# Optimization experiments

Measured on AMD Instinct MI355X. Metric: run time of the kernel, lower is better.

Reference implementation:

```python
import jax, jax.numpy as jnp
import numpy as np

NEG = -1e9
EPS = 1e-5


def _layernorm(x, g, b):
    m = x.mean(-1, keepdims=True)
    v = ((x - m) ** 2).mean(-1, keepdims=True)
    return (x - m) / jnp.sqrt(v + EPS) * g + b


def _layer(h_aug, H_inc, mask_neg, W1, W1_hat, ctx1, W2, W2_hat, W3, g, b):
    # h_aug: (T, H), H_inc/mask_neg: (T, E)
    H = h_aug.shape[-1]
    scale = 1.0 / jnp.sqrt(jnp.asarray(H, h_aug.dtype))
    # Stage 1: node -> hyperedge attention
    proj_hat = h_aug @ W1_hat.T                       # (T, H)
    raw = (proj_hat * ctx1).sum(-1) * scale           # (T,)
    score = raw[:, None] + mask_neg                   # (T, E)
    alpha = jax.nn.softmax(score, axis=0) * H_inc     # (T, E)
    hyper = alpha.T @ (h_aug @ W1.T)                  # (E, H)
    # Stage 2: hyperedge -> node attention
    proj2_hat = hyper @ W2_hat.T                      # (E, H)
    score_ne = (h_aug @ W3.T) @ proj2_hat.T * scale + mask_neg  # (T, E)
    beta = jax.nn.softmax(score_ne, axis=1) * H_inc   # (T, E)
    out = beta @ (hyper @ W2.T)                       # (T, H)
    return _layernorm(out + h_aug, g, b)


def reference(node_emb, H_inc, membership, W1, W1_hat, ctx1, W2, W2_hat, W3, ln_g, ln_b, region_init):
    B, N, H = node_emb.shape
    R = region_init.shape[0]
    L = W1.shape[0]
    mask_neg = jnp.where(H_inc == 0, NEG, 0.0).astype(node_emb.dtype)
    counts = jax.ops.segment_sum(jnp.ones((N,), node_emb.dtype), membership, num_segments=R)
    safe_counts = jnp.maximum(counts, 1.0)

    def per_sample(h):  # h: (N, H)
        sums = jax.ops.segment_sum(h, membership, num_segments=R)     # (R, H)
        reg = jnp.where(counts[:, None] > 0, sums / safe_counts[:, None], 0.0)
        reg = reg + region_init
        h_aug = jnp.concatenate([h, reg], axis=0)                     # (N+R, H)
        for l in range(L):
            h_aug = _layer(h_aug, H_inc, mask_neg, W1[l], W1_hat[l], ctx1[l],
                           W2[l], W2_hat[l], W3[l], ln_g[l], ln_b[l])
        return h_aug[:N]

    return jax.vmap(per_sample)(node_emb)


def setup_inputs() -> dict:
    key = jax.random.key(0)
    ks = jax.random.split(key, 12)
    B, N, R, E, H, L = 4, 8000, 16, 1024, 128, 2
    T = N + R
    w_std = 1.0 / np.sqrt(H)
    node_emb = jax.random.normal(ks[0], (B, N, H), dtype=jnp.float32)
    H_inc = (jax.random.uniform(ks[1], (T, E)) < 0.05).astype(jnp.float32)
    membership = jax.random.randint(ks[2], (N,), 0, R, dtype=jnp.int32)
    W1 = jax.random.normal(ks[3], (L, H, H), dtype=jnp.float32) * w_std
    W1_hat = jax.random.normal(ks[4], (L, H, H), dtype=jnp.float32) * w_std
    ctx1 = jax.random.normal(ks[5], (L, H), dtype=jnp.float32) * 0.02
    W2 = jax.random.normal(ks[6], (L, H, H), dtype=jnp.float32) * w_std
    W2_hat = jax.random.normal(ks[7], (L, H, H), dtype=jnp.float32) * w_std
    W3 = jax.random.normal(ks[8], (L, H, H), dtype=jnp.float32) * w_std
    ln_g = jnp.ones((L, H), dtype=jnp.float32)
    ln_b = jnp.zeros((L, H), dtype=jnp.float32)
    region_init = jax.random.normal(ks[9], (R, H), dtype=jnp.float32) * 0.02
    return {"node_emb": node_emb, "H_inc": H_inc, "membership": membership,
            "W1": W1, "W1_hat": W1_hat, "ctx1": ctx1, "W2": W2, "W2_hat": W2_hat,
            "W3": W3, "ln_g": ln_g, "ln_b": ln_b, "region_init": region_init}
```

## Files before the change

### kernel.cpp

```cpp
#include <hip/hip_runtime.h>

#define HD 128
#define CAPE 768
#define MAXR 16
#define NB_RS 128
#define KSTR 136
#define VSTR 72

typedef unsigned short u16;
typedef unsigned long long u64;
typedef __attribute__((ext_vector_type(8))) short bf16x8;
typedef __attribute__((ext_vector_type(4))) float f32x4;
typedef __attribute__((ext_vector_type(4))) unsigned u32x4;

__device__ inline float b2f(unsigned u){ return __uint_as_float(u << 16); }
__device__ inline u16 f2b(float x){
  unsigned u = __float_as_uint(x);
  return (u16)((u + 0x7fffu + ((u >> 16) & 1u)) >> 16);
}

__device__ inline float waveSum(float v){ for(int o=32;o;o>>=1) v += __shfl_down(v,o); return v; }
__device__ inline float waveMax(float v){ for(int o=32;o;o>>=1) v = fmaxf(v,__shfl_down(v,o)); return v; }

__device__ inline float blockSum128(float v, float* red){
  int j = threadIdx.x;
  float s = waveSum(v);
  __syncthreads();
  if ((j & 63) == 0) red[j >> 6] = s;
  __syncthreads();
  return red[0] + red[1];
}
__device__ inline float blockMax128(float v, float* red){
  int j = threadIdx.x;
  float s = waveMax(v);
  __syncthreads();
  if ((j & 63) == 0) red[j >> 6] = s;
  __syncthreads();
  return fmaxf(red[0], red[1]);
}

__global__ void k_count(const int* __restrict__ memb, int N, int* __restrict__ counts){
  __shared__ int h[64];
  int tid = threadIdx.x;
  if (tid < 64) h[tid] = 0;
  __syncthreads();
  for (int t = blockIdx.x*blockDim.x + tid; t < N; t += gridDim.x*blockDim.x)
    atomicAdd(&h[memb[t]], 1);
  __syncthreads();
  if (tid < 64){ int v = h[tid]; if (v) atomicAdd(&counts[tid], v); }
}

__global__ __launch_bounds__(128) void k_regsum_fast(const float* __restrict__ node,
                        const int* __restrict__ memb, int N, int R,
                        float* __restrict__ partials){
  int b = blockIdx.y, j = threadIdx.x, blk = blockIdx.x;
  int nb = gridDim.x;
  int per = (N + nb - 1) / nb;
  int t0 = blk * per;
  int t1 = t0 + per; if (t1 > N) t1 = N;
  float acc[MAXR];
  #pragma unroll
  for (int i = 0; i < MAXR; ++i) acc[i] = 0.f;
  const float* base = node + (long)b*N*HD + j;
  for (int t = t0; t < t1; ++t){
    float v = base[(long)t*HD];
    int r = memb[t];
    #pragma unroll
    for (int i = 0; i < MAXR; ++i) acc[i] += (i == r) ? v : 0.f;
  }
  float* dst = partials + ((long)(b*nb + blk)*R)*HD + j;
  #pragma unroll
  for (int i = 0; i < MAXR; ++i)
    if (i < R) dst[(long)i*HD] = acc[i];
}

__global__ void k_regsum_lds(const float* __restrict__ node, const int* __restrict__ memb,
                             int N, int R, float* __restrict__ partials, int nb){
  extern __shared__ float acc[];
  int b = blockIdx.y, j = threadIdx.x;
  for (int r = 0; r < R; ++r) acc[r*HD + j] = 0.f;
  int per = (N + gridDim.x - 1) / gridDim.x;
  int t0 = blockIdx.x * per;
  int t1 = t0 + per; if (t1 > N) t1 = N;
  for (int t = t0; t < t1; ++t){
    int r = memb[t];
    acc[r*HD + j] += node[((long)b*N + t)*HD + j];
  }
  for (int r = 0; r < R; ++r)
    atomicAdd(&partials[((long)(b*nb)*R + r)*HD + j], acc[r*HD + j]);
}

__global__ void k_regfin(const float* __restrict__ partials, int nb, int redN,
                         const int* __restrict__ counts,
                         const float* __restrict__ rinit, float* __restrict__ h_aug,
                         int N, int R, int T, int B){
  int i = blockIdx.x*blockDim.x + threadIdx.x;
  if (i >= B*R*HD) return;
  int j = i % HD; int r = (i/HD) % R; int b = i/(HD*R);
  float s = 0.f;
  for (int blk = 0; blk < redN; ++blk)
    s += partials[((long)(b*nb + blk)*R + r)*HD + j];
  int c = counts[r];
  float v = (c > 0) ? s / (float)c : 0.f;
  v += rinit[r*HD + j];
  h_aug[((long)b*T + N + r)*HD + j] = v;
}

__global__ __launch_bounds__(128) void k_copyraw(const float* __restrict__ node,
                      const float* __restrict__ v, float* __restrict__ h_aug,
                      float* __restrict__ raw, int N, int T, float scale){
  int t = blockIdx.x, b = blockIdx.y, j = threadIdx.x;
  __shared__ float red[2];
  long rowb = (long)b*T + t;
  float x;
  if (t < N){ x = node[((long)b*N + t)*HD + j]; h_aug[rowb*HD + j] = x; }
  else      { x = h_aug[rowb*HD + j]; }
  float s = blockSum128(x * v[j], red);
  if (j == 0) raw[rowb] = s * scale;
}

__global__ __launch_bounds__(256) void k_maskbuild(const float* __restrict__ Hinc, int E, int MW,
                        u64* __restrict__ maskw){
  int t = blockIdx.x;
  int wv = threadIdx.x >> 6, lane = threadIdx.x & 63;
  const float* hrow = Hinc + (long)t*E;
  for (int w = wv; w < MW; w += 4){
    int e = w*64 + lane;
    bool f = (e < E) && (hrow[e] != 0.f);
    u64 mk = __ballot(f);
    if (lane == 0) maskw[(long)t*MW + w] = mk;
  }
}

__global__ __launch_bounds__(256) void k_colbuild2(const u64* __restrict__ maskw, int T, int MW,
                           u16* __restrict__ colidx, int* __restrict__ colcnt){
  int e = blockIdx.x;
  int w = e >> 6, bit = e & 63;
  int j = threadIdx.x;
  int lane = j & 63, wv = j >> 6;
  __shared__ int wsum[4];
  int c = 0;
  for (int base = 0; base < T; base += 256){
    int t = base + j;
    bool f = (t < T) && ((maskw[(long)t*MW + w] >> bit) & 1ull);
    u64 mk = __ballot(f);
    if (lane == 0) wsum[wv] = __popcll(mk);
    __syncthreads();
    int pre = 0;
    #pragma unroll
    for (int k = 0; k < 4; ++k) pre += (k < wv) ? wsum[k] : 0;
    int tot = wsum[0] + wsum[1] + wsum[2] + wsum[3];
    if (f){
      int pos = c + pre + (int)__popcll(mk & ((1ull << lane) - 1ull));
      if (pos < CAPE) colidx[(long)e*CAPE + pos] = (u16)t;
    }
    c += tot;
    __syncthreads();
  }
  if (j == 0) colcnt[e] = (c < CAPE) ? c : CAPE;
}

__global__ void k_ctxv(const float* __restrict__ ctx1, const float* __restrict__ W1h,
                       float* __restrict__ v){
  int l = blockIdx.x, k = threadIdx.x;
  float a = 0.f;
  for (int j = 0; j < HD; ++j) a += ctx1[l*HD + j] * W1h[((long)l*HD + j)*HD + k];
  v[l*HD + k] = a;
}

__global__ void k_mm128(const float* __restrict__ W2h, const float* __restrict__ W3,
                        float* __restrict__ MqT){
  int n = blockIdx.x, l = blockIdx.y, k = threadIdx.x;
  const float* A = W2h + (long)l*HD*HD;
  const float* Bm = W3 + (long)l*HD*HD;
  float s = 0.f;
  for (int j = 0; j < HD; ++j) s += A[(long)j*HD + n] * Bm[(long)j*HD + k];
  MqT[((long)l*HD + n)*HD + k] = s;
}

__global__ __launch_bounds__(256) void k_gemmM(const float* __restrict__ A,
                       const float* __restrict__ Wa, const float* __restrict__ Wb,
                       u16* __restrict__ Cb16, float* __restrict__ Cf32, int M, int zbase){
  int isB = ((blockIdx.y + zbase) == 0) ? 1 : 0;
  const float* W = isB ? Wa : Wb;
  __shared__ __align__(16) u16 Ws[128][KSTR];
  __shared__ __align__(16) u16 As[64][KSTR];
  int tid = threadIdx.x;
  int row0 = blockIdx.x * 64;
  for (int i = tid; i < 128*128; i += 256){
    int r = i >> 7, c = i & 127;
    Ws[r][c] = f2b(W[(long)r*HD + c]);
  }
  for (int i = tid; i < 64*128; i += 256){
    int r = i >> 7, c = i & 127;
    int gr = row0 + r;
    As[r][c] = (gr < M) ? f2b(A[(long)gr*HD + c]) : (u16)0;
  }
  __syncthreads();

  int wave = tid >> 6, lane = tid & 63;
  int wr0 = wave * 16;
  int frow = lane & 15;
  int koff = (lane >> 4) * 8;
  f32x4 acc[8];
  #pragma unroll
  for (int f = 0; f < 8; ++f) acc[f] = (f32x4){0.f,0.f,0.f,0.f};

  #pragma unroll
  for (int ks = 0; ks < 4; ++ks){
    int kc = ks*32 + koff;
    bf16x8 av = *(const bf16x8*)&As[wr0 + frow][kc];
    #pragma unroll
    for (int f = 0; f < 8; ++f){
      bf16x8 bv = *(const bf16x8*)&Ws[f*16 + frow][kc];
      acc[f] = __builtin_amdgcn_mfma_f32_16x16x32_bf16(av, bv, acc[f], 0, 0, 0);
    }
  }

  int orow = wr0 + (lane >> 4) * 4;
  #pragma unroll
  for (int f = 0; f < 8; ++f){
    int col = f*16 + frow;
    #pragma unroll
    for (int i = 0; i < 4; ++i){
      int gr = row0 + orow + i;
      if (gr < M){
        if (isB) Cb16[(long)gr*HD + col] = f2b(acc[f][i]);
        else     Cf32[(long)gr*HD + col] = acc[f][i];
      }
    }
  }
}

__global__ __launch_bounds__(256) void k_gemmW2T(const float* __restrict__ W2,
                       const u16* __restrict__ hyb, u16* __restrict__ hw2t, int E){
  int b = blockIdx.y;
  int e0 = blockIdx.x * 64;
  __shared__ __align__(16) u16 As[128][KSTR];
  __shared__ __align__(16) u16 Bs[64][KSTR];
  int tid = threadIdx.x;
  for (int i = tid; i < 128*128; i += 256){
    int r = i >> 7, c = i & 127;
    As[r][c] = f2b(W2[(long)r*HD + c]);
  }
  {
    int er = tid >> 2, q = (tid & 3)*32;
    if (e0 + er < E){
      const uint4* src = (const uint4*)(hyb + ((long)b*E + e0 + er)*HD + q);
      uint4 w0 = src[0], w1 = src[1], w2 = src[2], w3 = src[3];
      *(uint4*)&Bs[er][q]    = w0;
      *(uint4*)&Bs[er][q+8]  = w1;
      *(uint4*)&Bs[er][q+16] = w2;
      *(uint4*)&Bs[er][q+24] = w3;
    } else {
      uint4 z = {0,0,0,0};
      *(uint4*)&Bs[er][q] = z; *(uint4*)&Bs[er][q+8] = z;
      *(uint4*)&Bs[er][q+16] = z; *(uint4*)&Bs[er][q+24] = z;
    }
  }
  __syncthreads();
  int wv = tid >> 6, lane = tid & 63;
  int lc = lane & 15, lg = lane >> 4;
  f32x4 acc[2][4];
  #pragma unroll
  for (int mt=0;mt<2;++mt)
    #pragma unroll
    for (int nf=0;nf<4;++nf) acc[mt][nf] = (f32x4){0.f,0.f,0.f,0.f};
  #pragma unroll
  for (int mt=0;mt<2;++mt){
    int hr = wv*32 + mt*16 + lc;
    #pragma unroll
    for (int ks=0;ks<4;++ks){
      bf16x8 av = *(const bf16x8*)&As[hr][ks*32 + lg*8];
      #pragma unroll
      for (int nf=0;nf<4;++nf){
        bf16x8 bv = *(const bf16x8*)&Bs[nf*16+lc][ks*32 + lg*8];
        acc[mt][nf] = __builtin_amdgcn_mfma_f32_16x16x32_bf16(av, bv, acc[mt][nf], 0,0,0);
      }
    }
  }
  #pragma unroll
  for (int mt=0;mt<2;++mt){
    #pragma unroll
    for (int nf=0;nf<4;++nf){
      #pragma unroll
      for (int i=0;i<4;++i){
        int h = wv*32 + mt*16 + lg*4 + i;
        int e = e0 + nf*16 + lc;
        if (e < E) hw2t[((long)b*HD + h)*E + e] = f2b(acc[mt][nf][i]);
      }
    }
  }
}

__global__ __launch_bounds__(128) void k_edge(int swz, const float* __restrict__ raw,
                      const u16* __restrict__ proj1b,
                      const int* __restrict__ colcnt, const u16* __restrict__ colidx,
                      u16* __restrict__ hyb, int T, int E){
  int bi = blockIdx.x;
  int b, e;
  if (swz){ int x = bi & 7; b = x >> 1; e = ((bi >> 3) << 1) | (x & 1); }
  else    { b = bi / E; e = bi - b*E; }
  int j = threadIdx.x;
  __shared__ float red[2];
  __shared__ float wls[CAPE];
  __shared__ int   tls[CAPE];
  int c = colcnt[e]; if (c > CAPE) c = CAPE;
  const u16* ci = colidx + (long)e*CAPE;
  const float* rawb = raw + (long)b*T;
  long orow = ((long)b*E + e)*HD + j;
  if (c <= 0){ hyb[orow] = 0; return; }
  float lm = -1e30f;
  for (int i = j; i < c; i += 128){
    int t = ci[i];
    float v = rawb[t];
    tls[i] = t;
    wls[i] = v;
    lm = fmaxf(lm, v);
  }
  float m = blockMax128(lm, red);
  float lz = 0.f;
  for (int i = j; i < c; i += 128){
    float w = __expf(wls[i] - m);
    wls[i] = w;
    lz += w;
  }
  float Z = blockSum128(lz, red);
  float invZ = 1.f / Z;
  const u16* pb = proj1b + (long)b*T*HD + j;
  float a0=0.f,a1=0.f,a2=0.f,a3=0.f;
  int i = 0;
  for (; i + 4 <= c; i += 4){
    a0 += wls[i]   * b2f(pb[(long)tls[i]  *HD]);
    a1 += wls[i+1] * b2f(pb[(long)tls[i+1]*HD]);
    a2 += wls[i+2] * b2f(pb[(long)tls[i+2]*HD]);
    a3 += wls[i+3] * b2f(pb[(long)tls[i+3]*HD]);
  }
  for (; i < c; ++i) a0 += wls[i] * b2f(pb[(long)tls[i]*HD]);
  hyb[orow] = f2b(((a0+a1)+(a2+a3)) * invZ);
}

__global__ __launch_bounds__(256) void k_flash(
      const float* __restrict__ qt, const u16* __restrict__ hyb, const u16* __restrict__ hw2t,
      const u64* __restrict__ maskw,
      const float* __restrict__ lng, const float* __restrict__ lnb,
      const float* __restrict__ vnext, float* __restrict__ rawnext, int writeRaw,
      float* __restrict__ h_aug, float* __restrict__ out,
      int T, int E, int N, int writeOut, float scale){
  int b = blockIdx.y;
  int t0 = blockIdx.x * 64;
  int tid = threadIdx.x;
  int wv = tid >> 6, lane = tid & 63;
  int lc = lane & 15, lg = lane >> 4;

  __shared__ __align__(16) u16 Ks[64][KSTR];
  __shared__ __align__(16) u16 Vs[128][VSTR];

  int qrow = t0 + wv*16 + lc;
  bf16x8 qf[4];
  if (qrow < T){
    const float* qr = qt + ((long)b*T + qrow)*HD + lg*8;
    #pragma unroll
    for (int ks = 0; ks < 4; ++ks){
      const float4* q4 = (const float4*)(qr + ks*32);
      float4 a = q4[0], cc = q4[1];
      bf16x8 v;
      v[0]=(short)f2b(a.x);  v[1]=(short)f2b(a.y);  v[2]=(short)f2b(a.z);  v[3]=(short)f2b(a.w);
      v[4]=(short)f2b(cc.x); v[5]=(short)f2b(cc.y); v[6]=(short)f2b(cc.z); v[7]=(short)f2b(cc.w);
      qf[ks] = v;
    }
  } else {
    #pragma unroll
    for (int ks = 0; ks < 4; ++ks) qf[ks] = (bf16x8){0,0,0,0,0,0,0,0};
  }

  float m_s = -1e30f, l_s = 0.f;
  f32x4 Oa[8];
  #pragma unroll
  for (int f=0;f<8;++f) Oa[f] = (f32x4){0.f,0.f,0.f,0.f};

  const u16* hyB = hyb + (long)b*E*HD;
  const u16* vtB = hw2t + (long)b*HD*E;
  int MW = (E + 63) >> 6;
  int ntile = (E + 63) / 64;

  int kr = tid >> 2, kq = (tid & 3)*32;
  int vh = tid >> 1, vo = (tid & 1)*32;

  uint4 kreg0, kreg1, kreg2, kreg3, vreg0, vreg1, vreg2, vreg3;
  const uint4 zz = make_uint4(0u,0u,0u,0u);

  {
    int e0 = 0;
    if (e0 + kr < E){
      const uint4* s = (const uint4*)(hyB + (long)(e0+kr)*HD + kq);
      kreg0=s[0]; kreg1=s[1]; kreg2=s[2]; kreg3=s[3];
    } else { kreg0=zz; kreg1=zz; kreg2=zz; kreg3=zz; }
    if (e0 + vo + 31 < E){
      const uint4* s = (const uint4*)(vtB + (long)vh*E + e0 + vo);
      vreg0=s[0]; vreg1=s[1]; vreg2=s[2]; vreg3=s[3];
    } else {
      union { uint4 v[4]; u16 s[32]; } u;
      #pragma unroll
      for (int k=0;k<32;++k){ int e=e0+vo+k; u.s[k] = (e<E)? vtB[(long)vh*E+e] : (u16)0; }
      vreg0=u.v[0]; vreg1=u.v[1]; vreg2=u.v[2]; vreg3=u.v[3];
    }
  }

  for (int et = 0; et < ntile; ++et){
    *(uint4*)&Ks[kr][kq]    = kreg0;
    *(uint4*)&Ks[kr][kq+8]  = kreg1;
    *(uint4*)&Ks[kr][kq+16] = kreg2;
    *(uint4*)&Ks[kr][kq+24] = kreg3;
    {
      int eb0 = vo;        int ne0 = eb0>>4; int ka0 = (ne0>>1)*32 + ((eb0>>2)&3)*8 + (ne0&1)*4;
      int eb1 = vo + 8;    int ne1 = eb1>>4; int ka1 = (ne1>>1)*32 + ((eb1>>2)&3)*8 + (ne1&1)*4;
      int eb2 = vo + 16;   int ne2 = eb2>>4; int ka2 = (ne2>>1)*32 + ((eb2>>2)&3)*8 + (ne2&1)*4;
      int eb3 = vo + 24;   int ne3 = eb3>>4; int ka3 = (ne3>>1)*32 + ((eb3>>2)&3)*8 + (ne3&1)*4;
      *(uint2*)&Vs[vh][ka0]   = make_uint2(vreg0.x, vreg0.y);
      *(uint2*)&Vs[vh][ka0+8] = make_uint2(vreg0.z, vreg0.w);
      *(uint2*)&Vs[vh][ka1]   = make_uint2(vreg1.x, vreg1.y);
      *(uint2*)&Vs[vh][ka1+8] = make_uint2(vreg1.z, vreg1.w);
      *(uint2*)&Vs[vh][ka2]   = make_uint2(vreg2.x, vreg2.y);
      *(uint2*)&Vs[vh][ka2+8] = make_uint2(vreg2.z, vreg2.w);
      *(uint2*)&Vs[vh][ka3]   = make_uint2(vreg3.x, vreg3.y);
      *(uint2*)&Vs[vh][ka3+8] = make_uint2(vreg3.z, vreg3.w);
    }
    __syncthreads();
    if (et + 1 < ntile){
      int e0 = (et+1)*64;
      if (e0 + kr < E){
        const uint4* s = (const uint4*)(hyB + (long)(e0+kr)*HD + kq);
        kreg0=s[0]; kreg1=s[1]; kreg2=s[2]; kreg3=s[3];
      } else { kreg0=zz; kreg1=zz; kreg2=zz; kreg3=zz; }
      if (e0 + vo + 31 < E){
        const uint4* s = (const uint4*)(vtB + (long)vh*E + e0 + vo);
        vreg0=s[0]; vreg1=s[1]; vreg2=s[2]; vreg3=s[3];
      } else {
        union { uint4 v[4]; u16 s[32]; } u;
        #pragma unroll
        for (int k=0;k<32;++k){ int e=e0+vo+k; u.s[k] = (e<E)? vtB[(long)vh*E+e] : (u16)0; }
        vreg0=u.v[0]; vreg1=u.v[1]; vreg2=u.v[2]; vreg3=u.v[3];
      }
    }

    u64 mw = (qrow < T) ? maskw[(long)qrow*MW + et] : 0ull;

    f32x4 accS[4];
    #pragma unroll
    for (int ne=0;ne<4;++ne) accS[ne] = (f32x4){0.f,0.f,0.f,0.f};
    __builtin_amdgcn_s_setprio(1);
    #pragma unroll
    for (int ks=0;ks<4;++ks){
      #pragma unroll
      for (int ne=0;ne<4;++ne){
        bf16x8 kv = *(const bf16x8*)&Ks[ne*16+lc][ks*32 + lg*8];
        accS[ne] = __builtin_amdgcn_mfma_f32_16x16x32_bf16(kv, qf[ks], accS[ne], 0,0,0);
      }
    }
    __builtin_amdgcn_s_setprio(0);

    unsigned lo = (unsigned)mw, hi = (unsigned)(mw >> 32);
    unsigned nib[4];
    nib[0] = (lo >> (lg*4)) & 0xFu;
    nib[1] = (lo >> (16 + lg*4)) & 0xFu;
    nib[2] = (hi >> (lg*4)) & 0xFu;
    nib[3] = (hi >> (16 + lg*4)) & 0xFu;

    float p[4][4];
    float mx = -1e30f;
    #pragma unroll
    for (int ne=0;ne<4;++ne){
      #pragma unroll
      for (int r=0;r<4;++r){
        float s = ((nib[ne] >> r) & 1u) ? accS[ne][r]*scale : -1e30f;
        p[ne][r] = s;
        mx = fmaxf(mx, s);
      }
    }
    mx = fmaxf(mx, __shfl_xor(mx, 16));
    mx = fmaxf(mx, __shfl_xor(mx, 32));
    float mn = fmaxf(m_s, mx);
    float corr = __expf(m_s - mn);
    m_s = mn;
    float ls = 0.f;
    #pragma unroll
    for (int ne=0;ne<4;++ne){
      #pragma unroll
      for (int r=0;r<4;++r){
        float pv = __expf(p[ne][r] - mn);
        p[ne][r] = pv;
        ls += pv;
      }
    }
    ls += __shfl_xor(ls, 16);
    ls += __shfl_xor(ls, 32);
    l_s = l_s*corr + ls;

    float corrO[4];
    #pragma unroll
    for (int i=0;i<4;++i) corrO[i] = __shfl(corr, lg*4 + i, 16);
    #pragma unroll
    for (int f=0;f<8;++f){
      #pragma unroll
      for (int i=0;i<4;++i) Oa[f][i] *= corrO[i];
    }

    unsigned pk00, pk01, pk10, pk11, pk20, pk21, pk30, pk31;
    asm("v_cvt_pk_bf16_f32 %0, %1, %2" : "=v"(pk00) : "v"(p[0][0]), "v"(p[0][1]));
    asm("v_cvt_pk_bf16_f32 %0, %1, %2" : "=v"(pk01) : "v"(p[0][2]), "v"(p[0][3]));
    asm("v_cvt_pk_bf16_f32 %0, %1, %2" : "=v"(pk10) : "v"(p[1][0]), "v"(p[1][1]));
    asm("v_cvt_pk_bf16_f32 %0, %1, %2" : "=v"(pk11) : "v"(p[1][2]), "v"(p[1][3]));
    asm("v_cvt_pk_bf16_f32 %0, %1, %2" : "=v"(pk20) : "v"(p[2][0]), "v"(p[2][1]));
    asm("v_cvt_pk_bf16_f32 %0, %1, %2" : "=v"(pk21) : "v"(p[2][2]), "v"(p[2][3]));
    asm("v_cvt_pk_bf16_f32 %0, %1, %2" : "=v"(pk30) : "v"(p[3][0]), "v"(p[3][1]));
    asm("v_cvt_pk_bf16_f32 %0, %1, %2" : "=v"(pk31) : "v"(p[3][2]), "v"(p[3][3]));

    __builtin_amdgcn_s_setprio(1);
    {
      u32x4 w0v = { pk00, pk01, pk10, pk11 };
      bf16x8 pa0 = __builtin_bit_cast(bf16x8, w0v);
      #pragma unroll
      for (int f=0;f<8;++f){
        bf16x8 vb = *(const bf16x8*)&Vs[f*16+lc][lg*8];
        Oa[f] = __builtin_amdgcn_mfma_f32_16x16x32_bf16(pa0, vb, Oa[f], 0,0,0);
      }
      u32x4 w1v = { pk20, pk21, pk30, pk31 };
      bf16x8 pa1 = __builtin_bit_cast(bf16x8, w1v);
      #pragma unroll
      for (int f=0;f<8;++f){
        bf16x8 vb = *(const bf16x8*)&Vs[f*16+lc][32 + lg*8];
        Oa[f] = __builtin_amdgcn_mfma_f32_16x16x32_bf16(pa1, vb, Oa[f], 0,0,0);
      }
    }
    __builtin_amdgcn_s_setprio(0);
    __syncthreads();
  }

  float invl = (l_s > 0.f) ? 1.f/l_s : 0.f;
  #pragma unroll
  for (int i=0;i<4;++i){
    int t = t0 + wv*16 + lg*4 + i;
    if (t >= T) continue;
    long rowb = (long)b*T + t;
    float inv = __shfl(invl, lg*4 + i, 16);
    float xv[8];
    float sm = 0.f;
    #pragma unroll
    for (int f=0;f<8;++f){
      float o = Oa[f][i]*inv;
      float h = h_aug[rowb*HD + f*16+lc];
      xv[f] = o + h;
      sm += xv[f];
    }
    sm += __shfl_xor(sm,1); sm += __shfl_xor(sm,2);
    sm += __shfl_xor(sm,4); sm += __shfl_xor(sm,8);
    float mean = sm * (1.f/HD);
    float vr = 0.f;
    #pragma unroll
    for (int f=0;f<8;++f){ float d = xv[f]-mean; vr += d*d; }
    vr += __shfl_xor(vr,1); vr += __shfl_xor(vr,2);
    vr += __shfl_xor(vr,4); vr += __shfl_xor(vr,8);
    float rstd = rsqrtf(vr*(1.f/HD) + 1e-5f);
    float rsum = 0.f;
    #pragma unroll
    for (int f=0;f<8;++f){
      int col = f*16+lc;
      float y = (xv[f]-mean)*rstd*lng[col] + lnb[col];
      if (writeOut){ if (t < N) out[((long)b*N + t)*HD + col] = y; }
      else h_aug[rowb*HD + col] = y;
      rsum += y * vnext[col];
    }
    rsum += __shfl_xor(rsum,1); rsum += __shfl_xor(rsum,2);
    rsum += __shfl_xor(rsum,4); rsum += __shfl_xor(rsum,8);
    if (writeRaw && lc == 0) rawnext[rowb] = rsum * scale;
  }
}

extern "C" void kernel_launch(void* const* d_in, const int* in_sizes, int n_in,
                              void* d_out, int out_size, void* d_ws, size_t ws_size,
                              hipStream_t stream) {
  const float* node_emb = (const float*)d_in[0];
  const float* Hinc     = (const float*)d_in[1];
  const int*   memb     = (const int*)d_in[2];
  const float* W1       = (const float*)d_in[3];
  const float* W1h      = (const float*)d_in[4];
  const float* ctx1     = (const float*)d_in[5];
  const float* W2       = (const float*)d_in[6];
  const float* W2h      = (const float*)d_in[7];
  const float* W3       = (const float*)d_in[8];
  const float* lng      = (const float*)d_in[9];
  const float* lnb      = (const float*)d_in[10];
  const float* rinit    = (const float*)d_in[11];
  float* out = (float*)d_out;

  const int N  = in_sizes[2];
  const int Hd = in_sizes[3] / in_sizes[5];
  const int L  = in_sizes[5] / Hd;
  const int R  = in_sizes[11] / Hd;
  const int B  = in_sizes[0] / (N * Hd);
  const int T  = N + R;
  const int E  = in_sizes[1] / T;
  const int MW = (E + 63) / 64;
  const float scale = 1.0f / sqrtf((float)Hd);

  char* p = (char*)d_ws;
  auto carve = [&](size_t bytes){ char* r = p; p += (bytes + 255) & ~(size_t)255; return (void*)r; };
  float* h_aug  = (float*)carve((size_t)B*T*Hd*4);
  u16*   proj1b = (u16*)  carve((size_t)B*T*Hd*2);
  float* qt     = (float*)carve((size_t)B*T*Hd*4);
  u16*   hyb    = (u16*)  carve((size_t)B*E*Hd*2);
  u16*   hw2t   = (u16*)  carve((size_t)B*Hd*E*2);
  float* MqT    = (float*)carve((size_t)L*Hd*Hd*4);
  float* rawb   = (float*)carve((size_t)B*T*4);
  float* vbuf   = (float*)carve((size_t)L*Hd*4);
  u64*   maskw  = (u64*)  carve((size_t)T*MW*8);
  int* counts   = (int*)carve((size_t)R*4);
  int* col_cnt  = (int*)carve((size_t)E*4);
  u16* col_idx  = (u16*)carve((size_t)E*CAPE*2);

  float* partials = qt;

  hipMemsetAsync(counts, 0, (size_t)R*4, stream);

  k_count<<<32, 256, 0, stream>>>(memb, N, counts);

  int redN;
  if (R <= MAXR){
    k_regsum_fast<<<dim3(NB_RS, B), 128, 0, stream>>>(node_emb, memb, N, R, partials);
    redN = NB_RS;
  } else {
    hipMemsetAsync(partials, 0, (size_t)B*R*Hd*4, stream);
    k_regsum_lds<<<dim3(16, B), Hd, (size_t)R*Hd*4, stream>>>(node_emb, memb, N, R, partials, NB_RS);
    redN = 1;
  }
  int tot = B*R*Hd;
  k_regfin<<<(tot+255)/256, 256, 0, stream>>>(partials, NB_RS, redN, counts, rinit, h_aug, N, R, T, B);

  k_maskbuild<<<T, 256, 0, stream>>>(Hinc, E, MW, maskw);
  k_colbuild2<<<E, 256, 0, stream>>>(maskw, T, MW, col_idx, col_cnt);

  k_ctxv<<<L, Hd, 0, stream>>>(ctx1, W1h, vbuf);
  k_mm128<<<dim3(Hd, L), Hd, 0, stream>>>(W2h, W3, MqT);
  k_copyraw<<<dim3(T, B), 128, 0, stream>>>(node_emb, vbuf, h_aug, rawb, N, T, scale);

  int MT = B*T;
  int gTm = (MT + 63)/64;
  int gTf = (T + 63)/64;
  int gEt = (E + 63)/64;
  int swzE = (B == 4 && (E & 1) == 0) ? 1 : 0;
  for (int l = 0; l < L; ++l){
    size_t wo = (size_t)l*Hd*Hd;
    k_gemmM<<<dim3(gTm, 2), 256, 0, stream>>>(h_aug, W1 + wo, MqT + wo, proj1b, qt, MT, 0);
    k_edge<<<B*E, 128, 0, stream>>>(swzE, rawb, proj1b, col_cnt, col_idx, hyb, T, E);
    k_gemmW2T<<<dim3(gEt, B), 256, 0, stream>>>(W2 + wo, hyb, hw2t, E);
    int writeRaw = (l < L-1) ? 1 : 0;
    const float* vnext = vbuf + (size_t)((l+1 < L) ? (l+1) : l)*Hd;
    k_flash<<<dim3(gTf, B), 256, 0, stream>>>(qt, hyb, hw2t, maskw,
                                    lng + wo/Hd, lnb + wo/Hd,
                                    vnext, rawb, writeRaw,
                                    h_aug, out, T, E, N, (l == L-1) ? 1 : 0, scale);
  }
}
```

Before: 405.8 us.

## Split flash attention over hyperedge tiles and merge partials with layernorm

The flash kernel's hyperedge loop is split into two halves run as separate blocks (split-K), writing bf16 partial outputs plus per-row max and sum. A new merge kernel combines them and applies the residual add, layernorm and next-layer raw score. The split is meant to give the GPU more blocks to fill its compute units, since the grid was only about 500 blocks. Other changes: Q is stored in bf16 so it needs no conversion, the output rescale is skipped unless the running max grows by more than 8 (lazy rescaling), and the region-sum partial count is halved. The cost is an extra kernel launch, extra traffic for the partial outputs, and some precision loss from storing partials in bf16.

```diff
diff --git a/kernel.cpp b/kernel.cpp
--- a/kernel.cpp
+++ b/kernel.cpp
@@ -3,7 +3,7 @@
 #define HD 128
 #define CAPE 768
 #define MAXR 16
-#define NB_RS 128
+#define NB_RS 64
 #define KSTR 136
 #define VSTR 72
 
@@ -180,9 +180,9 @@
 
 __global__ __launch_bounds__(256) void k_gemmM(const float* __restrict__ A,
                        const float* __restrict__ Wa, const float* __restrict__ Wb,
-                       u16* __restrict__ Cb16, float* __restrict__ Cf32, int M, int zbase){
-  int isB = ((blockIdx.y + zbase) == 0) ? 1 : 0;
-  const float* W = isB ? Wa : Wb;
+                       u16* __restrict__ Ca, u16* __restrict__ Cb, int M){
+  const float* W = blockIdx.y ? Wb : Wa;
+  u16* C = blockIdx.y ? Cb : Ca;
   __shared__ __align__(16) u16 Ws[128][KSTR];
   __shared__ __align__(16) u16 As[64][KSTR];
   int tid = threadIdx.x;
@@ -224,10 +224,7 @@
     #pragma unroll
     for (int i = 0; i < 4; ++i){
       int gr = row0 + orow + i;
-      if (gr < M){
-        if (isB) Cb16[(long)gr*HD + col] = f2b(acc[f][i]);
-        else     Cf32[(long)gr*HD + col] = acc[f][i];
-      }
+      if (gr < M) C[(long)gr*HD + col] = f2b(acc[f][i]);
     }
   }
 }
@@ -340,14 +337,13 @@
   hyb[orow] = f2b(((a0+a1)+(a2+a3)) * invZ);
 }
 
-__global__ __launch_bounds__(256) void k_flash(
-      const float* __restrict__ qt, const u16* __restrict__ hyb, const u16* __restrict__ hw2t,
+__global__ __launch_bounds__(256) void k_flashp(
+      const u16* __restrict__ qtb, const u16* __restrict__ hyb, const u16* __restrict__ hw2t,
       const u64* __restrict__ maskw,
-      const float* __restrict__ lng, const float* __restrict__ lnb,
-      const float* __restrict__ vnext, float* __restrict__ rawnext, int writeRaw,
-      float* __restrict__ h_aug, float* __restrict__ out,
-      int T, int E, int N, int writeOut, float scale){
-  int b = blockIdx.y;
+      u16* __restrict__ Opart, float* __restrict__ mpart, float* __restrict__ lpart,
+      int T, int E, int half, float scale){
+  int b = blockIdx.y, Bc = gridDim.y;
+  int s = blockIdx.z, nsplit = gridDim.z;
   int t0 = blockIdx.x * 64;
   int tid = threadIdx.x;
   int wv = tid >> 6, lane = tid & 63;
@@ -356,19 +352,17 @@
   __shared__ __align__(16) u16 Ks[64][KSTR];
   __shared__ __align__(16) u16 Vs[128][VSTR];
 
+  int MW = (E + 63) >> 6;
+  int ntile = (E + 63) / 64;
+  int et0 = s * half;
+  int etend = (s == nsplit-1) ? ntile : ((s+1)*half < ntile ? (s+1)*half : ntile);
+
   int qrow = t0 + wv*16 + lc;
   bf16x8 qf[4];
   if (qrow < T){
-    const float* qr = qt + ((long)b*T + qrow)*HD + lg*8;
-    #pragma unroll
-    for (int ks = 0; ks < 4; ++ks){
-      const float4* q4 = (const float4*)(qr + ks*32);
-      float4 a = q4[0], cc = q4[1];
-      bf16x8 v;
-      v[0]=(short)f2b(a.x);  v[1]=(short)f2b(a.y);  v[2]=(short)f2b(a.z);  v[3]=(short)f2b(a.w);
-      v[4]=(short)f2b(cc.x); v[5]=(short)f2b(cc.y); v[6]=(short)f2b(cc.z); v[7]=(short)f2b(cc.w);
-      qf[ks] = v;
-    }
+    const u16* qr = qtb + ((long)b*T + qrow)*HD + lg*8;
+    #pragma unroll
+    for (int ks = 0; ks < 4; ++ks) qf[ks] = *(const bf16x8*)(qr + ks*32);
   } else {
     #pragma unroll
     for (int ks = 0; ks < 4; ++ks) qf[ks] = (bf16x8){0,0,0,0,0,0,0,0};
@@ -381,8 +375,6 @@
 
   const u16* hyB = hyb + (long)b*E*HD;
   const u16* vtB = hw2t + (long)b*HD*E;
-  int MW = (E + 63) >> 6;
-  int ntile = (E + 63) / 64;
 
   int kr = tid >> 2, kq = (tid & 3)*32;
   int vh = tid >> 1, vo = (tid & 1)*32;
@@ -390,15 +382,15 @@
   uint4 kreg0, kreg1, kreg2, kreg3, vreg0, vreg1, vreg2, vreg3;
   const uint4 zz = make_uint4(0u,0u,0u,0u);
 
-  {
-    int e0 = 0;
+  if (et0 < etend){
+    int e0 = et0*64;
     if (e0 + kr < E){
-      const uint4* s = (const uint4*)(hyB + (long)(e0+kr)*HD + kq);
-      kreg0=s[0]; kreg1=s[1]; kreg2=s[2]; kreg3=s[3];
+      const uint4* sp = (const uint4*)(hyB + (long)(e0+kr)*HD + kq);
+      kreg0=sp[0]; kreg1=sp[1]; kreg2=sp[2]; kreg3=sp[3];
     } else { kreg0=zz; kreg1=zz; kreg2=zz; kreg3=zz; }
     if (e0 + vo + 31 < E){
-      const uint4* s = (const uint4*)(vtB + (long)vh*E + e0 + vo);
-      vreg0=s[0]; vreg1=s[1]; vreg2=s[2]; vreg3=s[3];
+      const uint4* sp = (const uint4*)(vtB + (long)vh*E + e0 + vo);
+      vreg0=sp[0]; vreg1=sp[1]; vreg2=sp[2]; vreg3=sp[3];
     } else {
       union { uint4 v[4]; u16 s[32]; } u;
       #pragma unroll
@@ -407,7 +399,7 @@
     }
   }
 
-  for (int et = 0; et < ntile; ++et){
+  for (int et = et0; et < etend; ++et){
     *(uint4*)&Ks[kr][kq]    = kreg0;
     *(uint4*)&Ks[kr][kq+8]  = kreg1;
     *(uint4*)&Ks[kr][kq+16] = kreg2;
@@ -427,15 +419,15 @@
       *(uint2*)&Vs[vh][ka3+8] = make_uint2(vreg3.z, vreg3.w);
     }
     __syncthreads();
-    if (et + 1 < ntile){
+    if (et + 1 < etend){
       int e0 = (et+1)*64;
       if (e0 + kr < E){
-        const uint4* s = (const uint4*)(hyB + (long)(e0+kr)*HD + kq);
-        kreg0=s[0]; kreg1=s[1]; kreg2=s[2]; kreg3=s[3];
+        const uint4* sp = (const uint4*)(hyB + (long)(e0+kr)*HD + kq);
+        kreg0=sp[0]; kreg1=sp[1]; kreg2=sp[2]; kreg3=sp[3];
       } else { kreg0=zz; kreg1=zz; kreg2=zz; kreg3=zz; }
       if (e0 + vo + 31 < E){
-        const uint4* s = (const uint4*)(vtB + (long)vh*E + e0 + vo);
-        vreg0=s[0]; vreg1=s[1]; vreg2=s[2]; vreg3=s[3];
+        const uint4* sp = (const uint4*)(vtB + (long)vh*E + e0 + vo);
+        vreg0=sp[0]; vreg1=sp[1]; vreg2=sp[2]; vreg3=sp[3];
       } else {
         union { uint4 v[4]; u16 s[32]; } u;
         #pragma unroll
@@ -468,27 +460,40 @@
     nib[3] = (hi >> (16 + lg*4)) & 0xFu;
 
     float p[4][4];
-    float mx = -1e30f;
+    float mx = -3e30f;
     #pragma unroll
     for (int ne=0;ne<4;++ne){
       #pragma unroll
       for (int r=0;r<4;++r){
-        float s = ((nib[ne] >> r) & 1u) ? accS[ne][r]*scale : -1e30f;
-        p[ne][r] = s;
-        mx = fmaxf(mx, s);
+        float sv = ((nib[ne] >> r) & 1u) ? accS[ne][r]*scale : -3e30f;
+        p[ne][r] = sv;
+        mx = fmaxf(mx, sv);
       }
     }
     mx = fmaxf(mx, __shfl_xor(mx, 16));
     mx = fmaxf(mx, __shfl_xor(mx, 32));
-    float mn = fmaxf(m_s, mx);
-    float corr = __expf(m_s - mn);
-    m_s = mn;
+
+    float corr = 1.f;
+    if (!__all(mx <= m_s + 8.f)){
+      float mn = fmaxf(m_s, mx);
+      corr = __expf(m_s - mn);
+      m_s = mn;
+      float corrO[4];
+      #pragma unroll
+      for (int i=0;i<4;++i) corrO[i] = __shfl(corr, lg*4 + i, 16);
+      #pragma unroll
+      for (int f=0;f<8;++f){
+        #pragma unroll
+        for (int i=0;i<4;++i) Oa[f][i] *= corrO[i];
+      }
+    }
+
     float ls = 0.f;
     #pragma unroll
     for (int ne=0;ne<4;++ne){
       #pragma unroll
       for (int r=0;r<4;++r){
-        float pv = __expf(p[ne][r] - mn);
+        float pv = __expf(p[ne][r] - m_s);
         p[ne][r] = pv;
         ls += pv;
       }
@@ -496,15 +501,6 @@
     ls += __shfl_xor(ls, 16);
     ls += __shfl_xor(ls, 32);
     l_s = l_s*corr + ls;
-
-    float corrO[4];
-    #pragma unroll
-    for (int i=0;i<4;++i) corrO[i] = __shfl(corr, lg*4 + i, 16);
-    #pragma unroll
-    for (int f=0;f<8;++f){
-      #pragma unroll
-      for (int i=0;i<4;++i) Oa[f][i] *= corrO[i];
-    }
 
     unsigned pk00, pk01, pk10, pk11, pk20, pk21, pk30, pk31;
     asm("v_cvt_pk_bf16_f32 %0, %1, %2" : "=v"(pk00) : "v"(p[0][0]), "v"(p[0][1]));
@@ -537,43 +533,58 @@
     __syncthreads();
   }
 
-  float invl = (l_s > 0.f) ? 1.f/l_s : 0.f;
+  u16* Ob = Opart + (((long)s*Bc + b)*T)*HD;
   #pragma unroll
   for (int i=0;i<4;++i){
     int t = t0 + wv*16 + lg*4 + i;
     if (t >= T) continue;
-    long rowb = (long)b*T + t;
-    float inv = __shfl(invl, lg*4 + i, 16);
-    float xv[8];
-    float sm = 0.f;
-    #pragma unroll
-    for (int f=0;f<8;++f){
-      float o = Oa[f][i]*inv;
-      float h = h_aug[rowb*HD + f*16+lc];
-      xv[f] = o + h;
-      sm += xv[f];
-    }
-    sm += __shfl_xor(sm,1); sm += __shfl_xor(sm,2);
-    sm += __shfl_xor(sm,4); sm += __shfl_xor(sm,8);
-    float mean = sm * (1.f/HD);
-    float vr = 0.f;
-    #pragma unroll
-    for (int f=0;f<8;++f){ float d = xv[f]-mean; vr += d*d; }
-    vr += __shfl_xor(vr,1); vr += __shfl_xor(vr,2);
-    vr += __shfl_xor(vr,4); vr += __shfl_xor(vr,8);
-    float rstd = rsqrtf(vr*(1.f/HD) + 1e-5f);
-    float rsum = 0.f;
-    #pragma unroll
-    for (int f=0;f<8;++f){
-      int col = f*16+lc;
-      float y = (xv[f]-mean)*rstd*lng[col] + lnb[col];
-      if (writeOut){ if (t < N) out[((long)b*N + t)*HD + col] = y; }
-      else h_aug[rowb*HD + col] = y;
-      rsum += y * vnext[col];
-    }
-    rsum += __shfl_xor(rsum,1); rsum += __shfl_xor(rsum,2);
-    rsum += __shfl_xor(rsum,4); rsum += __shfl_xor(rsum,8);
-    if (writeRaw && lc == 0) rawnext[rowb] = rsum * scale;
+    #pragma unroll
+    for (int f=0;f<8;++f)
+      Ob[(long)t*HD + f*16 + lc] = f2b(Oa[f][i]);
+  }
+  if (lg == 0 && qrow < T){
+    long mlrow = ((long)s*Bc + b)*T + qrow;
+    mpart[mlrow] = m_s;
+    lpart[mlrow] = l_s;
+  }
+}
+
+__global__ __launch_bounds__(128) void k_merge(
+      const u16* __restrict__ Opart, const float* __restrict__ mpart, const float* __restrict__ lpart,
+      int nsplit,
+      const float* __restrict__ lng, const float* __restrict__ lnb,
+      const float* __restrict__ vnext, float* __restrict__ rawnext, int writeRaw,
+      float* __restrict__ h_aug, float* __restrict__ out,
+      int T, int N, int writeOut, float scale){
+  int t = blockIdx.x, b = blockIdx.y, j = threadIdx.x;
+  int Bc = gridDim.y;
+  __shared__ float red[2];
+  long r0 = ((long)b)*T + t;
+  long r1 = ((long)Bc + b)*T + t;
+  float m0 = mpart[r0], l0 = lpart[r0];
+  float m1 = (nsplit > 1) ? mpart[r1] : -1e30f;
+  float l1 = (nsplit > 1) ? lpart[r1] : 0.f;
+  float M = fmaxf(m0, m1);
+  float c0 = __expf(m0 - M), c1 = __expf(m1 - M);
+  float l = l0*c0 + l1*c1;
+  float inv = (l > 0.f) ? 1.f/l : 0.f;
+  float o = b2f(Opart[r0*HD + j]) * c0;
+  if (nsplit > 1) o += b2f(Opart[r1*HD + j]) * c1;
+  o *= inv;
+  long rowb = (long)b*T + t;
+  float x = o + h_aug[rowb*HD + j];
+  float mean = blockSum128(x, red) * (1.f/HD);
+  float d = x - mean;
+  float var = blockSum128(d*d, red) * (1.f/HD);
+  float y = d * rsqrtf(var + 1e-5f) * lng[j] + lnb[j];
+  if (writeOut){
+    if (t < N) out[((long)b*N + t)*HD + j] = y;
+  } else {
+    h_aug[rowb*HD + j] = y;
+  }
+  if (writeRaw){
+    float s = blockSum128(y * vnext[j], red);
+    if (j == 0) rawnext[rowb] = s * scale;
   }
 }
 
@@ -608,7 +619,7 @@
   auto carve = [&](size_t bytes){ char* r = p; p += (bytes + 255) & ~(size_t)255; return (void*)r; };
   float* h_aug  = (float*)carve((size_t)B*T*Hd*4);
   u16*   proj1b = (u16*)  carve((size_t)B*T*Hd*2);
-  float* qt     = (float*)carve((size_t)B*T*Hd*4);
+  u16*   qtb    = (u16*)  carve((size_t)B*T*Hd*2);
   u16*   hyb    = (u16*)  carve((size_t)B*E*Hd*2);
   u16*   hw2t   = (u16*)  carve((size_t)B*Hd*E*2);
   float* MqT    = (float*)carve((size_t)L*Hd*Hd*4);
@@ -618,8 +629,17 @@
   int* counts   = (int*)carve((size_t)R*4);
   int* col_cnt  = (int*)carve((size_t)E*4);
   u16* col_idx  = (u16*)carve((size_t)E*CAPE*2);
-
-  float* partials = qt;
+  float* mpart  = (float*)carve((size_t)2*B*T*4);
+  float* lpart  = (float*)carve((size_t)2*B*T*4);
+
+  size_t used = (size_t)(p - (char*)d_ws);
+  size_t rem  = (ws_size > used) ? (ws_size - used) : 0;
+  size_t needP  = (size_t)B*NB_RS*R*Hd*4;
+  size_t needO2 = (size_t)2*B*T*Hd*2;
+  size_t need2 = needP > needO2 ? needP : needO2;
+  int SPLIT = (rem >= need2) ? 2 : 1;
+  float* partials = (float*)p;
+  u16*   Opart    = (u16*)p;
 
   hipMemsetAsync(counts, 0, (size_t)R*4, stream);
 
@@ -648,17 +668,21 @@
   int gTm = (MT + 63)/64;
   int gTf = (T + 63)/64;
   int gEt = (E + 63)/64;
+  int ntile = (E + 63)/64;
+  int half = (ntile + SPLIT - 1)/SPLIT;
   int swzE = (B == 4 && (E & 1) == 0) ? 1 : 0;
   for (int l = 0; l < L; ++l){
     size_t wo = (size_t)l*Hd*Hd;
-    k_gemmM<<<dim3(gTm, 2), 256, 0, stream>>>(h_aug, W1 + wo, MqT + wo, proj1b, qt, MT, 0);
+    k_gemmM<<<dim3(gTm, 2), 256, 0, stream>>>(h_aug, W1 + wo, MqT + wo, proj1b, qtb, MT);
     k_edge<<<B*E, 128, 0, stream>>>(swzE, rawb, proj1b, col_cnt, col_idx, hyb, T, E);
     k_gemmW2T<<<dim3(gEt, B), 256, 0, stream>>>(W2 + wo, hyb, hw2t, E);
+    k_flashp<<<dim3(gTf, B, SPLIT), 256, 0, stream>>>(qtb, hyb, hw2t, maskw,
+                                    Opart, mpart, lpart, T, E, half, scale);
     int writeRaw = (l < L-1) ? 1 : 0;
     const float* vnext = vbuf + (size_t)((l+1 < L) ? (l+1) : l)*Hd;
-    k_flash<<<dim3(gTf, B), 256, 0, stream>>>(qt, hyb, hw2t, maskw,
+    k_merge<<<dim3(T, B), 128, 0, stream>>>(Opart, mpart, lpart, SPLIT,
                                     lng + wo/Hd, lnb + wo/Hd,
                                     vnext, rawb, writeRaw,
-                                    h_aug, out, T, E, N, (l == L-1) ? 1 : 0, scale);
-  }
-}
+                                    h_aug, out, T, N, (l == L-1) ? 1 : 0, scale);
+  }
+}
```

Result: slower. 430.8 us (+6.1%).
